# Optimization experiments

Measured on AMD Instinct MI355X. Metric: run time of the kernel, lower is better.

The kernel has to match this reference:

```python
import jax, jax.numpy as jnp
import numpy as np

EPS = 1e-5  # BatchNorm2d default eps


def _binarize_ste(x):
    """Forward: sign(x). Backward: hardtanh STE (grad 1 where |x|<=1, else 0)."""
    xc = jnp.clip(x, -1.0, 1.0)
    return xc + jax.lax.stop_gradient(jnp.sign(x) - xc)


def setup_inputs() -> dict:
    key = jax.random.key(0)
    k1, k2, k3, k4 = jax.random.split(key, 4)
    x = jax.random.normal(k1, (32, 256, 32, 32), dtype=jnp.float32)
    # BatchNorm affine params (affine=True)
    gamma = 1.0 + 0.1 * jax.random.normal(k2, (256,), dtype=jnp.float32)
    beta = 0.1 * jax.random.normal(k3, (256,), dtype=jnp.float32)
    # Conv weight, OIHW, bias=False
    W = 0.05 * jax.random.normal(k4, (256, 256, 3, 3), dtype=jnp.float32)
    return {"x": x, "gamma": gamma, "beta": beta, "W": W}


def reference(x, gamma, beta, W):
    # BatchNorm2d, training-mode batch statistics over (N, H, W) per channel
    mean = jnp.mean(x, axis=(0, 2, 3), keepdims=True)
    var = jnp.var(x, axis=(0, 2, 3), keepdims=True)
    xn = (x - mean) * jax.lax.rsqrt(var + EPS)
    xn = xn * gamma[None, :, None, None] + beta[None, :, None, None]
    # Conv2d_1w1a: binarize activations and weights (sign fwd / STE bwd), then conv
    a = _binarize_ste(xn)
    wb = _binarize_ste(W)
    out = jax.lax.conv_general_dilated(
        a, wb,
        window_strides=(1, 1),
        padding=((1, 1), (1, 1)),
        dimension_numbers=("NCHW", "OIHW", "NCHW"),
    )
    return out
```

## Files before the change

### kernel.cpp

```cpp
#include <hip/hip_runtime.h>
#include <hip/hip_bf16.h>


#define NIMG 32
#define C    256
#define K    256

typedef int v4i  __attribute__((ext_vector_type(4)));
typedef int v16i __attribute__((ext_vector_type(16)));

#define AHT_IMG 295936
#define AHT_KB  36992
#define AHT_ROW 1088


__global__ __launch_bounds__(256) void k_stats_packw(
    const float* __restrict__ x, const float* __restrict__ W,
    double2* __restrict__ partials, char* __restrict__ wfrag) {
  int bx = blockIdx.x;
  int tid = threadIdx.x;
  if (bx >= 2048) {
    int k = bx - 2048, c = tid;
    const float* src = W + ((size_t)k * 256 + c) * 9;
    char* dst = wfrag + (size_t)(c >> 4) * 4096 + k * 16 + (c & 15);
    #pragma unroll
    for (int t = 0; t < 9; ++t)
      dst[(size_t)t * 65536] = (src[t] > 0.0f) ? (char)1 : (char)-1;
    return;
  }
  int c = bx >> 3, grp = bx & 7;
  double s = 0.0, sq = 0.0;
  #pragma unroll
  for (int ni = 0; ni < 4; ++ni) {
    int n = grp * 4 + ni;
    const float* p = x + (size_t)n * (C * 1024) + (size_t)c * 1024;
    float4 v = ((const float4*)p)[tid];
    s += (double)v.x + (double)v.y + (double)v.z + (double)v.w;
    sq += (double)v.x * v.x + (double)v.y * v.y
        + (double)v.z * v.z + (double)v.w * v.w;
  }
  for (int o = 32; o > 0; o >>= 1) {
    s += __shfl_down(s, o);
    sq += __shfl_down(sq, o);
  }
  __shared__ double ls[4], lq[4];
  if ((tid & 63) == 0) { ls[tid >> 6] = s; lq[tid >> 6] = sq; }
  __syncthreads();
  if (tid == 0) {
    double2 r;
    r.x = ls[0] + ls[1] + ls[2] + ls[3];
    r.y = lq[0] + lq[1] + lq[2] + lq[3];
    partials[c * 8 + grp] = r;
  }
}

__global__ __launch_bounds__(256) void k_packa_i8(
    const float* __restrict__ x, const double2* __restrict__ partials,
    const float* __restrict__ gamma, const float* __restrict__ beta,
    char* __restrict__ aHT) {
  __shared__ float lf[32 * 257];
  __shared__ float lthr[256];
  __shared__ unsigned lfl[256];
  int y = blockIdx.x, n = blockIdx.y, tid = threadIdx.x;

  {
    double S = 0.0, Q = 0.0;
    #pragma unroll
    for (int g = 0; g < 8; ++g) {
      double2 p = partials[tid * 8 + g];
      S += p.x; Q += p.y;
    }
    const double N = 32768.0;
    double mean = S / N;
    double var = Q / N - mean * mean;
    double rs = 1.0 / sqrt(var + 1e-5);
    double gm = (double)gamma[tid];
    double bt = (double)beta[tid];
    float t;
    unsigned flip;
    if (gm == 0.0) {
      t = (bt > 0.0) ? -3.0e38f : 3.0e38f;
      flip = 0u;
    } else {
      t = (float)(mean - bt / (rs * gm));
      flip = (gm < 0.0) ? 1u : 0u;
    }
    lthr[tid] = t;
    lfl[tid] = flip;
  }

  #pragma unroll
  for (int it = 0; it < 8; ++it) {
    int c = it * 32 + (tid >> 3), q = tid & 7;
    float4 v = *(const float4*)(x + (size_t)n * 262144 + (size_t)c * 1024
                                + y * 32 + q * 4);
    lf[(q * 4 + 0) * 257 + c] = v.x;
    lf[(q * 4 + 1) * 257 + c] = v.y;
    lf[(q * 4 + 2) * 257 + c] = v.z;
    lf[(q * 4 + 3) * 257 + c] = v.w;
  }
  __syncthreads();
  int xl = tid & 31, cb = tid >> 5;
  unsigned wds[8];
  #pragma unroll
  for (int g = 0; g < 8; ++g) {
    unsigned wv = 0;
    #pragma unroll
    for (int jj = 0; jj < 4; ++jj) {
      int c = cb * 32 + g * 4 + jj;
      float v = lf[xl * 257 + c];
      unsigned bit = ((v > lthr[c]) ? 1u : 0u) ^ lfl[c];
      unsigned byte = bit ? 0x01u : 0xFFu;
      wv |= byte << (8 * jj);
    }
    wds[g] = wv;
  }
  char* dst = aHT + ((size_t)n * 8 + cb) * AHT_KB
            + (size_t)(y + 1) * AHT_ROW + (size_t)(xl + 1) * 32;
  uint4 u0, u1;
  u0.x = wds[0]; u0.y = wds[1]; u0.z = wds[2]; u0.w = wds[3];
  u1.x = wds[4]; u1.y = wds[5]; u1.z = wds[6]; u1.w = wds[7];
  *(uint4*)dst = u0;
  *((uint4*)dst + 1) = u1;

  uint4 z; z.x = 0; z.y = 0; z.z = 0; z.w = 0;
  if (xl < 2) {
    char* hz = aHT + ((size_t)n * 8 + cb) * AHT_KB
             + (size_t)(y + 1) * AHT_ROW + (size_t)(xl * 33) * 32;
    *(uint4*)hz = z;
    *((uint4*)hz + 1) = z;
  }
  if (y == 0 || y == 31) {
    int row = (y == 0) ? 0 : 33;
    for (int idx = tid; idx < 272; idx += 256) {
      int kb = idx / 34, xx = idx % 34;
      char* hz = aHT + ((size_t)n * 8 + kb) * AHT_KB
               + (size_t)row * AHT_ROW + (size_t)xx * 32;
      *(uint4*)hz = z;
      *((uint4*)hz + 1) = z;
    }
  }
}

__global__ __launch_bounds__(512) void k_conv_mfma(
    const char* __restrict__ aHT, const char* __restrict__ wfrag,
    float* __restrict__ out) {
  __shared__ uint4 As4[3264];
  char* As = (char*)As4;
  int tid = threadIdx.x;
  int lane = tid & 63, w = tid >> 6;
  int nh = w & 3, mb = w >> 2;
  int bx = blockIdx.x;
  int lb = (bx & 7) * 32 + (bx >> 3);
  int n = lb >> 3, ys = lb & 7;
  int y0 = ys * 4;
  int yw = y0 + mb * 2;
  int xl = lane & 31, hi = lane >> 5;

  {
    const char* aImg = aHT + (size_t)n * AHT_IMG;
    for (int e = tid; e < 3264; e += 512) {
      int px = e % 34;
      int q = e / 34;
      int hs = q & 1;
      int q2 = q >> 1;
      int rl = q2 % 6;
      int kb = q2 / 6;
      const char* g = aImg + (size_t)kb * AHT_KB
                    + (size_t)(y0 + rl) * AHT_ROW + px * 32 + hs * 16;
      *(v4i*)(As + (size_t)e * 16) = *(const v4i*)g;
    }
  }
  __syncthreads();

  const char* wB = wfrag + hi * 4096 + (nh * 64 + xl) * 16;
  int aBase = (mb * 2 + 1) * 1088 + hi * 544 + (xl + 1) * 16;

  v16i a00 = {0}, a01 = {0}, a10 = {0}, a11 = {0};
  v4i c0, c1, c2, c3, d0, d1, d2, d3, e0, e1, e2, e3;

  #define LOADB(P, R0, R1, R2, R3)                                            \
    { const char* bp_ = wB + (size_t)(P) * 16384;                             \
      R0 = *(const v4i*)(bp_);                                                \
      R1 = *(const v4i*)(bp_ + 512);                                          \
      R2 = *(const v4i*)(bp_ + 8192);                                         \
      R3 = *(const v4i*)(bp_ + 8704); }

  LOADB(0, c0, c1, c2, c3);
  LOADB(1, d0, d1, d2, d3);

  for (int p = 0; p < 36; ++p) {
    if (p < 34) LOADB(p + 2, e0, e1, e2, e3);
    int tap = p >> 2, kb0 = (p & 3) * 2;
    int dy = tap / 3 - 1, dx = tap % 3 - 1;
    int ab = aBase + kb0 * 6528 + dy * 1088 + dx * 16;
    v4i Ar0k0 = *(const v4i*)(As + ab);
    v4i Ar1k0 = *(const v4i*)(As + ab + 1088);
    v4i Ar0k1 = *(const v4i*)(As + ab + 6528);
    v4i Ar1k1 = *(const v4i*)(As + ab + 6528 + 1088);
    a00 = __builtin_amdgcn_mfma_i32_32x32x32_i8(Ar0k0, c0, a00, 0, 0, 0);
    a01 = __builtin_amdgcn_mfma_i32_32x32x32_i8(Ar0k0, c1, a01, 0, 0, 0);
    a10 = __builtin_amdgcn_mfma_i32_32x32x32_i8(Ar1k0, c0, a10, 0, 0, 0);
    a11 = __builtin_amdgcn_mfma_i32_32x32x32_i8(Ar1k0, c1, a11, 0, 0, 0);
    a00 = __builtin_amdgcn_mfma_i32_32x32x32_i8(Ar0k1, c2, a00, 0, 0, 0);
    a01 = __builtin_amdgcn_mfma_i32_32x32x32_i8(Ar0k1, c3, a01, 0, 0, 0);
    a10 = __builtin_amdgcn_mfma_i32_32x32x32_i8(Ar1k1, c2, a10, 0, 0, 0);
    a11 = __builtin_amdgcn_mfma_i32_32x32x32_i8(Ar1k1, c3, a11, 0, 0, 0);
    if (p < 35) {
      c0 = d0; c1 = d1; c2 = d2; c3 = d3;
      d0 = e0; d1 = e1; d2 = e2; d3 = e3;
    }
  }
  #undef LOADB

  size_t ob0 = (size_t)n * 262144 + (size_t)(nh * 64 + xl) * 1024
             + (size_t)yw * 32 + 4 * hi;
  #pragma unroll
  for (int r = 0; r < 2; ++r) {
    #pragma unroll
    for (int nb = 0; nb < 2; ++nb) {
      v16i av = (r == 0) ? (nb == 0 ? a00 : a01) : (nb == 0 ? a10 : a11);
      float* obp = out + ob0 + (size_t)nb * 32768 + r * 32;
      #pragma unroll
      for (int q = 0; q < 4; ++q) {
        float4 f;
        f.x = (float)av[q * 4 + 0];
        f.y = (float)av[q * 4 + 1];
        f.z = (float)av[q * 4 + 2];
        f.w = (float)av[q * 4 + 3];
        *(float4*)(obp + 8 * q) = f;
      }
    }
  }
}


__global__ __launch_bounds__(256) void k_stats_part_fb(
    const float* __restrict__ x, double2* __restrict__ partials) {
  int grp = blockIdx.x;
  int c = blockIdx.y;
  int tid = threadIdx.x;
  double s = 0.0, sq = 0.0;
  #pragma unroll
  for (int ni = 0; ni < 4; ++ni) {
    int n = grp * 4 + ni;
    const float* p = x + (size_t)n * (C * 1024) + (size_t)c * 1024;
    float4 v = ((const float4*)p)[tid];
    s += (double)v.x + (double)v.y + (double)v.z + (double)v.w;
    sq += (double)v.x * v.x + (double)v.y * v.y
        + (double)v.z * v.z + (double)v.w * v.w;
  }
  for (int o = 32; o > 0; o >>= 1) {
    s += __shfl_down(s, o);
    sq += __shfl_down(sq, o);
  }
  __shared__ double ls[4], lq[4];
  if ((tid & 63) == 0) { ls[tid >> 6] = s; lq[tid >> 6] = sq; }
  __syncthreads();
  if (tid == 0) {
    double2 r;
    r.x = ls[0] + ls[1] + ls[2] + ls[3];
    r.y = lq[0] + lq[1] + lq[2] + lq[3];
    partials[c * 8 + grp] = r;
  }
}

__global__ __launch_bounds__(256) void k_packw_corr_final(
    const float* __restrict__ W, const double2* __restrict__ partials,
    const float* __restrict__ gamma, const float* __restrict__ beta,
    unsigned* __restrict__ wp, int* __restrict__ corr,
    unsigned* __restrict__ zp, float* __restrict__ t_out,
    unsigned* __restrict__ flip_out) {
  int bk = blockIdx.x;
  int tid = threadIdx.x;
  if (bk == 256) {
    int c = tid;
    double S = 0.0, Q = 0.0;
    #pragma unroll
    for (int g = 0; g < 8; ++g) {
      double2 p = partials[c * 8 + g];
      S += p.x; Q += p.y;
    }
    const double N = 32768.0;
    double mean = S / N;
    double var = Q / N - mean * mean;
    double rs = 1.0 / sqrt(var + 1e-5);
    double g = (double)gamma[c];
    double b = (double)beta[c];
    float t;
    unsigned flip;
    if (g == 0.0) {
      t = (b > 0.0) ? -3.0e38f : 3.0e38f;
      flip = 0u;
    } else {
      t = (float)(mean - b / (rs * g));
      flip = (g < 0.0) ? 1u : 0u;
    }
    t_out[c] = t;
    flip_out[c] = flip;
    return;
  }
  int k = bk;
  __shared__ unsigned lw[72];
  float w[9];
  const float* src = W + (size_t)k * 2304 + (size_t)tid * 9;
  #pragma unroll
  for (int t = 0; t < 9; ++t) w[t] = src[t];
  int lane = tid & 63, wv = tid >> 6;
  #pragma unroll
  for (int t = 0; t < 9; ++t) {
    unsigned long long m = __ballot(w[t] > 0.0f);
    if (lane == 0) {
      lw[t * 8 + 2 * wv] = (unsigned)m;
      lw[t * 8 + 2 * wv + 1] = (unsigned)(m >> 32);
    }
  }
  __syncthreads();
  if (tid < 72) wp[(size_t)k * 72 + tid] = lw[tid];
  if (tid >= 128 && tid < 144) {
    int cls = tid - 128;
    int sum = 0;
    #pragma unroll
    for (int t = 0; t < 9; ++t) {
      int dy = t / 3 - 1, dx = t % 3 - 1;
      bool inv = (((cls & 1) && dx == -1) || ((cls & 2) && dx == 1) ||
                  ((cls & 4) && dy == -1) || ((cls & 8) && dy == 1));
      if (inv) {
        #pragma unroll
        for (int j = 0; j < 8; ++j) sum += __popc(lw[t * 8 + j]);
      }
    }
    corr[k * 16 + cls] = sum;
  }
  if (bk == 0 && tid >= 192 && tid < 200) zp[tid - 192] = 0u;
}

__global__ __launch_bounds__(256) void k_packa_bits(
    const float* __restrict__ x, const float* __restrict__ t,
    const unsigned* __restrict__ flip, unsigned* __restrict__ ap) {
  int n = blockIdx.y;
  int p0 = blockIdx.x * 64;
  int pix = threadIdx.x & 63;
  int q = threadIdx.x >> 6;
  unsigned w0 = 0, w1 = 0;
  const float* xb = x + (size_t)n * (C * 1024) + p0 + pix;
  #pragma unroll
  for (int i = 0; i < 64; ++i) {
    int c = q * 64 + i;
    float tv = t[c];
    unsigned fl = flip[c];
    float v = xb[(size_t)c * 1024];
    unsigned bit = ((v > tv) ? 1u : 0u) ^ fl;
    if (i < 32) w0 |= bit << i;
    else        w1 |= bit << (i - 32);
  }
  uint2 st; st.x = w0; st.y = w1;
  *(uint2*)(ap + ((size_t)n * 1024 + p0 + pix) * 8 + q * 2) = st;
}

__global__ __launch_bounds__(256) void k_conv_pop(
    const unsigned* __restrict__ ap, const unsigned* __restrict__ wp,
    const int* __restrict__ corr, const unsigned* __restrict__ zp,
    float* __restrict__ out) {
  int n = blockIdx.z;
  int ystrip = blockIdx.y;
  int kc = blockIdx.x;
  int tid = threadIdx.x;
  int lane = tid & 63;
  int wave = tid >> 6;
  int y = ystrip * 8 + wave * 2 + (lane >> 5);
  int xx = lane & 31;
  int cls = (xx == 0 ? 1 : 0) | (xx == 31 ? 2 : 0) |
            (y == 0 ? 4 : 0) | (y == 31 ? 8 : 0);
  uint4 a0[9], a1[9];
  int nv = 0;
  const uint4* zp4 = (const uint4*)zp;
  #pragma unroll
  for (int t = 0; t < 9; ++t) {
    int dy = t / 3 - 1, dx = t % 3 - 1;
    int cy = y + dy, cx = xx + dx;
    bool valid = (cy >= 0) & (cy < 32) & (cx >= 0) & (cx < 32);
    nv += valid ? 1 : 0;
    const uint4* pa = valid
        ? (const uint4*)(ap + (((size_t)n * 32 + cy) * 32 + cx) * 8)
        : zp4;
    a0[t] = pa[0];
    a1[t] = pa[1];
  }
  int bias = nv << 8;
  float* ob = out + (size_t)n * (K * 1024) + (size_t)y * 32 + xx;
  for (int kk = 0; kk < 16; ++kk) {
    int k = kc * 16 + kk;
    const uint4* wq = (const uint4*)(wp + (size_t)k * 72);
    int s0 = 0, s1 = 0, s2 = 0, s3 = 0, s4 = 0, s5 = 0, s6 = 0, s7 = 0;
    #pragma unroll
    for (int t = 0; t < 9; ++t) {
      uint4 wa = wq[t * 2];
      uint4 wb = wq[t * 2 + 1];
      s0 += __popc(a0[t].x ^ wa.x);
      s1 += __popc(a0[t].y ^ wa.y);
      s2 += __popc(a0[t].z ^ wa.z);
      s3 += __popc(a0[t].w ^ wa.w);
      s4 += __popc(a1[t].x ^ wb.x);
      s5 += __popc(a1[t].y ^ wb.y);
      s6 += __popc(a1[t].z ^ wb.z);
      s7 += __popc(a1[t].w ^ wb.w);
    }
    int S = ((s0 + s1) + (s2 + s3)) + ((s4 + s5) + (s6 + s7));
    int tot = corr[(k << 4) + cls] - S;
    ob[(size_t)k * 1024] = (float)(bias + 2 * tot);
  }
}


extern "C" void kernel_launch(void* const* d_in, const int* in_sizes, int n_in,
                              void* d_out, int out_size, void* d_ws, size_t ws_size,
                              hipStream_t stream) {
  const float* x = (const float*)d_in[0];
  const float* gamma = (const float*)d_in[1];
  const float* beta = (const float*)d_in[2];
  const float* W = (const float*)d_in[3];
  float* out = (float*)d_out;
  char* ws = (char*)d_ws;

  const size_t NEED = 655360 + (size_t)NIMG * AHT_IMG;
  if (ws_size >= NEED) {
    double2* partials = (double2*)(ws + 4096);
    char* wfrag = ws + 36864;
    char* aHT = ws + 655360;

    k_stats_packw<<<2304, 256, 0, stream>>>(x, W, partials, wfrag);
    k_packa_i8<<<dim3(32, 32), 256, 0, stream>>>(x, partials, gamma, beta, aHT);
    k_conv_mfma<<<256, 512, 0, stream>>>(aHT, wfrag, out);
  } else {
    float* t = (float*)ws;
    unsigned* flip = (unsigned*)(ws + 1024);
    unsigned* wp = (unsigned*)(ws + 4096);
    unsigned* zp = (unsigned*)(ws + 77824);
    int* corr = (int*)(ws + 78336);
    double2* partials = (double2*)(ws + 98304);
    unsigned* ap = (unsigned*)(ws + 131072);

    k_stats_part_fb<<<dim3(8, 256), 256, 0, stream>>>(x, partials);
    k_packw_corr_final<<<257, 256, 0, stream>>>(W, partials, gamma, beta,
                                                wp, corr, zp, t, flip);
    k_packa_bits<<<dim3(16, 32), 256, 0, stream>>>(x, t, flip, ap);
    k_conv_pop<<<dim3(16, 4, 32), 256, 0, stream>>>(ap, wp, corr, zp, out);
  }
}
```

Before: 49.19 us.

## Split conv blocks into half-height tiles with deeper weight prefetch

The MFMA conv kernel now runs 512 blocks of 256 threads, each covering two output rows instead of four, which shrinks the LDS halo tile from 6 to 4 rows. The halo staging loop is unrolled with cheaper index math. The weight prefetch ring grows from two to three stages, held as an indexed register array inside a fully unrolled loop. The aim is more blocks across the CUs and better latency hiding. In exchange, the halo rows are loaded with proportionally more redundancy per block, and register pressure goes up.

```diff
diff --git a/kernel.cpp b/kernel.cpp
--- a/kernel.cpp
+++ b/kernel.cpp
@@ -142,79 +142,77 @@
   }
 }
 
-__global__ __launch_bounds__(512) void k_conv_mfma(
+__global__ __launch_bounds__(256) void k_conv_mfma(
     const char* __restrict__ aHT, const char* __restrict__ wfrag,
     float* __restrict__ out) {
-  __shared__ uint4 As4[3264];
+  __shared__ uint4 As4[2176];
   char* As = (char*)As4;
   int tid = threadIdx.x;
-  int lane = tid & 63, w = tid >> 6;
-  int nh = w & 3, mb = w >> 2;
+  int lane = tid & 63, nh = tid >> 6;
   int bx = blockIdx.x;
-  int lb = (bx & 7) * 32 + (bx >> 3);
-  int n = lb >> 3, ys = lb & 7;
-  int y0 = ys * 4;
-  int yw = y0 + mb * 2;
+  int lb = (bx & 7) * 64 + (bx >> 3);
+  int n = lb >> 4, ys = lb & 15;
+  int y0 = ys * 2;
   int xl = lane & 31, hi = lane >> 5;
 
   {
     const char* aImg = aHT + (size_t)n * AHT_IMG;
-    for (int e = tid; e < 3264; e += 512) {
-      int px = e % 34;
-      int q = e / 34;
-      int hs = q & 1;
-      int q2 = q >> 1;
-      int rl = q2 % 6;
-      int kb = q2 / 6;
-      const char* g = aImg + (size_t)kb * AHT_KB
-                    + (size_t)(y0 + rl) * AHT_ROW + px * 32 + hs * 16;
-      *(v4i*)(As + (size_t)e * 16) = *(const v4i*)g;
+    #pragma unroll
+    for (int it = 0; it < 9; ++it) {
+      int e = it * 256 + tid;
+      if (e < 2176) {
+        int q = e / 34, px = e - q * 34;
+        int hs = q & 1, q2 = q >> 1;
+        int rl = q2 & 3, kb = q2 >> 2;
+        const char* g = aImg + (size_t)kb * AHT_KB
+                      + (size_t)(y0 + rl) * AHT_ROW + px * 32 + hs * 16;
+        *(v4i*)(As + (size_t)e * 16) = *(const v4i*)g;
+      }
     }
   }
   __syncthreads();
 
   const char* wB = wfrag + hi * 4096 + (nh * 64 + xl) * 16;
-  int aBase = (mb * 2 + 1) * 1088 + hi * 544 + (xl + 1) * 16;
+  int aCol = (xl + 1) * 16 + hi * 544;
 
   v16i a00 = {0}, a01 = {0}, a10 = {0}, a11 = {0};
-  v4i c0, c1, c2, c3, d0, d1, d2, d3, e0, e1, e2, e3;
-
-  #define LOADB(P, R0, R1, R2, R3)                                            \
+  v4i B[3][4];
+
+  #define LOADB(P, S)                                                         \
     { const char* bp_ = wB + (size_t)(P) * 16384;                             \
-      R0 = *(const v4i*)(bp_);                                                \
-      R1 = *(const v4i*)(bp_ + 512);                                          \
-      R2 = *(const v4i*)(bp_ + 8192);                                         \
-      R3 = *(const v4i*)(bp_ + 8704); }
-
-  LOADB(0, c0, c1, c2, c3);
-  LOADB(1, d0, d1, d2, d3);
-
+      B[S][0] = *(const v4i*)(bp_);                                           \
+      B[S][1] = *(const v4i*)(bp_ + 512);                                     \
+      B[S][2] = *(const v4i*)(bp_ + 8192);                                    \
+      B[S][3] = *(const v4i*)(bp_ + 8704); }
+
+  LOADB(0, 0);
+  LOADB(1, 1);
+  LOADB(2, 2);
+
+  #pragma unroll
   for (int p = 0; p < 36; ++p) {
-    if (p < 34) LOADB(p + 2, e0, e1, e2, e3);
+    const int set = p % 3;
     int tap = p >> 2, kb0 = (p & 3) * 2;
     int dy = tap / 3 - 1, dx = tap % 3 - 1;
-    int ab = aBase + kb0 * 6528 + dy * 1088 + dx * 16;
+    int ab = (kb0 * 8 + (1 + dy) * 2) * 544 + aCol + dx * 16;
     v4i Ar0k0 = *(const v4i*)(As + ab);
     v4i Ar1k0 = *(const v4i*)(As + ab + 1088);
-    v4i Ar0k1 = *(const v4i*)(As + ab + 6528);
-    v4i Ar1k1 = *(const v4i*)(As + ab + 6528 + 1088);
-    a00 = __builtin_amdgcn_mfma_i32_32x32x32_i8(Ar0k0, c0, a00, 0, 0, 0);
-    a01 = __builtin_amdgcn_mfma_i32_32x32x32_i8(Ar0k0, c1, a01, 0, 0, 0);
-    a10 = __builtin_amdgcn_mfma_i32_32x32x32_i8(Ar1k0, c0, a10, 0, 0, 0);
-    a11 = __builtin_amdgcn_mfma_i32_32x32x32_i8(Ar1k0, c1, a11, 0, 0, 0);
-    a00 = __builtin_amdgcn_mfma_i32_32x32x32_i8(Ar0k1, c2, a00, 0, 0, 0);
-    a01 = __builtin_amdgcn_mfma_i32_32x32x32_i8(Ar0k1, c3, a01, 0, 0, 0);
-    a10 = __builtin_amdgcn_mfma_i32_32x32x32_i8(Ar1k1, c2, a10, 0, 0, 0);
-    a11 = __builtin_amdgcn_mfma_i32_32x32x32_i8(Ar1k1, c3, a11, 0, 0, 0);
-    if (p < 35) {
-      c0 = d0; c1 = d1; c2 = d2; c3 = d3;
-      d0 = e0; d1 = e1; d2 = e2; d3 = e3;
-    }
+    v4i Ar0k1 = *(const v4i*)(As + ab + 4352);
+    v4i Ar1k1 = *(const v4i*)(As + ab + 4352 + 1088);
+    a00 = __builtin_amdgcn_mfma_i32_32x32x32_i8(Ar0k0, B[set][0], a00, 0, 0, 0);
+    a01 = __builtin_amdgcn_mfma_i32_32x32x32_i8(Ar0k0, B[set][1], a01, 0, 0, 0);
+    a10 = __builtin_amdgcn_mfma_i32_32x32x32_i8(Ar1k0, B[set][0], a10, 0, 0, 0);
+    a11 = __builtin_amdgcn_mfma_i32_32x32x32_i8(Ar1k0, B[set][1], a11, 0, 0, 0);
+    a00 = __builtin_amdgcn_mfma_i32_32x32x32_i8(Ar0k1, B[set][2], a00, 0, 0, 0);
+    a01 = __builtin_amdgcn_mfma_i32_32x32x32_i8(Ar0k1, B[set][3], a01, 0, 0, 0);
+    a10 = __builtin_amdgcn_mfma_i32_32x32x32_i8(Ar1k1, B[set][2], a10, 0, 0, 0);
+    a11 = __builtin_amdgcn_mfma_i32_32x32x32_i8(Ar1k1, B[set][3], a11, 0, 0, 0);
+    if (p < 33) LOADB(p + 3, set);
   }
   #undef LOADB
 
   size_t ob0 = (size_t)n * 262144 + (size_t)(nh * 64 + xl) * 1024
-             + (size_t)yw * 32 + 4 * hi;
+             + (size_t)y0 * 32 + 4 * hi;
   #pragma unroll
   for (int r = 0; r < 2; ++r) {
     #pragma unroll
@@ -431,7 +429,7 @@
 
     k_stats_packw<<<2304, 256, 0, stream>>>(x, W, partials, wfrag);
     k_packa_i8<<<dim3(32, 32), 256, 0, stream>>>(x, partials, gamma, beta, aHT);
-    k_conv_mfma<<<256, 512, 0, stream>>>(aHT, wfrag, out);
+    k_conv_mfma<<<512, 256, 0, stream>>>(aHT, wfrag, out);
   } else {
     float* t = (float*)ws;
     unsigned* flip = (unsigned*)(ws + 1024);
```

New measurement: 56.62 us. +15.1%, slower.
